# Performance work log

Measured on AMD Instinct MI355X. Metric: run time of the kernel, lower is better.

The kernel has to match this reference:

```python
import jax, jax.numpy as jnp
import numpy as np

COST_CLASS = 1.0
COST_OBJECTNESS = 5.0
COST_GIOU = 2.0
COST_CENTER = 10.0

B, Q, G, C = 32, 1024, 64, 256


def _lsa(cost):
    """Exact rectangular linear sum assignment (Jonker-Volgenant shortest
    augmenting path, same algorithm as scipy.optimize.linear_sum_assignment).
    cost: (R, Cc) float64 numpy array. Returns (row_ind, col_ind), row_ind sorted."""
    transposed = cost.shape[0] > cost.shape[1]
    if transposed:
        cost = cost.T
    n, m = cost.shape
    u = np.zeros(n)
    v = np.zeros(m)
    col4row = np.full(n, -1, dtype=np.int64)
    row4col = np.full(m, -1, dtype=np.int64)
    for cur_row in range(n):
        shortest = np.full(m, np.inf)
        path = np.full(m, -1, dtype=np.int64)
        SC = np.zeros(m, dtype=bool)
        SR_rows = []
        min_val = 0.0
        i = cur_row
        sink = -1
        while sink == -1:
            SR_rows.append(i)
            idx = np.where(~SC)[0]
            r = min_val + cost[i, idx] - u[i] - v[idx]
            better = r < shortest[idx]
            upd = idx[better]
            shortest[upd] = r[better]
            path[upd] = i
            j = idx[np.argmin(shortest[idx])]
            min_val = shortest[j]
            SC[j] = True
            if row4col[j] == -1:
                sink = j
            else:
                i = row4col[j]
        # dual variable update
        u[cur_row] += min_val
        for irow in SR_rows:
            if irow != cur_row:
                u[irow] += min_val - shortest[col4row[irow]]
        v[SC] -= min_val - shortest[SC]
        # augment along the alternating path back to cur_row
        j = sink
        while True:
            i = path[j]
            row4col[j] = i
            col4row[i], j = j, col4row[i]
            if i == cur_row:
                break
    if transposed:
        order = np.argsort(col4row)
        return col4row[order], np.arange(n)[order]
    return np.arange(n), col4row


def setup_inputs() -> dict:
    key = jax.random.key(0)
    k1, k2, k3, k4, k5 = jax.random.split(key, 5)
    return {
        "sem_cls_prob": jax.random.uniform(k1, (B, Q, C), dtype=jnp.float32),
        "objectness_prob": jax.random.uniform(k2, (B, Q), dtype=jnp.float32),
        "center_dist": jax.random.uniform(k3, (B, Q, G), dtype=jnp.float32),
        "gious": jax.random.uniform(k4, (B, Q, G), dtype=jnp.float32),
        "nactual_gt": jax.random.randint(k5, (B,), 0, G, dtype=jnp.int64)
        if jax.config.jax_enable_x64 else jax.random.randint(k5, (B,), 0, G).astype(jnp.int32),
    }


def reference(sem_cls_prob, objectness_prob, center_dist, gious, nactual_gt):
    batchsize, nprop = objectness_prob.shape
    # class_mat == 0 in the original module
    final_cost = (COST_OBJECTNESS * (-objectness_prob[..., None])
                  + COST_CENTER * center_dist
                  + COST_GIOU * (-gious))  # [B, Q, G]
    cost_np = np.asarray(final_cost, dtype=np.float64)
    ngt = np.asarray(nactual_gt)
    per_prop_gt_inds = np.zeros((batchsize, nprop), dtype=np.int64)
    proposal_matched_mask = np.zeros((batchsize, nprop), dtype=np.float32)
    for b in range(batchsize):  # per-batch independent Hungarian (as in source)
        g = int(ngt[b])
        if g > 0:
            rows, cols = _lsa(cost_np[b, :, :g])
            per_prop_gt_inds[b, rows] = cols
            proposal_matched_mask[b, rows] = 1.0
    return jnp.asarray(per_prop_gt_inds), jnp.asarray(proposal_matched_mask)
```

## Files before the change

### kernel.cpp

```cpp
#include <hip/hip_runtime.h>
#include <math.h>

#define B_ 32
#define Q_ 1024
#define G_ 64
#define K16 16

typedef double v16d __attribute__((ext_vector_type(16)));
typedef float  v16f __attribute__((ext_vector_type(16)));
typedef int    v16i __attribute__((ext_vector_type(16)));

#define REP16(OP) OP(0,0) OP(1,1) OP(2,2) OP(3,3) OP(4,4) OP(5,5) OP(6,6) OP(7,7) \
                  OP(8,8) OP(9,9) OP(10,a) OP(11,b) OP(12,c) OP(13,d) OP(14,e) OP(15,f)
#define REP16A(OP,A) OP(A,0,0) OP(A,1,1) OP(A,2,2) OP(A,3,3) OP(A,4,4) OP(A,5,5) OP(A,6,6) OP(A,7,7) \
                     OP(A,8,8) OP(A,9,9) OP(A,10,a) OP(A,11,b) OP(A,12,c) OP(A,13,d) OP(A,14,e) OP(A,15,f)

#define ROR1 0x121
#define ROR2 0x122
#define ROR4 0x124
#define ROR8 0x128
#define BC15 0x142
#define BC31 0x143

template<int CTRL>
__device__ __forceinline__ double dpp_f64(double x) {
    union { double d; int i[2]; } a; a.d = x;
    union { int i[2]; double d; } r;
    r.i[0] = __builtin_amdgcn_update_dpp(a.i[0], a.i[0], CTRL, 0xF, 0xF, false);
    r.i[1] = __builtin_amdgcn_update_dpp(a.i[1], a.i[1], CTRL, 0xF, 0xF, false);
    return r.d;
}
template<int CTRL>
__device__ __forceinline__ int dpp_i32(int x) {
    return __builtin_amdgcn_update_dpp(x, x, CTRL, 0xF, 0xF, false);
}

__device__ __forceinline__ double readlane_f64(double x, int sl) {
    const int s = __builtin_amdgcn_readfirstlane(sl);
    union { double d; int i2[2]; } a; a.d = x;
    union { int i2[2]; double d; } r;
    r.i2[0] = __builtin_amdgcn_readlane(a.i2[0], s);
    r.i2[1] = __builtin_amdgcn_readlane(a.i2[1], s);
    return r.d;
}
__device__ __forceinline__ double readlane_f64c(double x, int sl) {
    union { double d; int i2[2]; } a; a.d = x;
    union { int i2[2]; double d; } r;
    r.i2[0] = __builtin_amdgcn_readlane(a.i2[0], sl);
    r.i2[1] = __builtin_amdgcn_readlane(a.i2[1], sl);
    return r.d;
}
__device__ __forceinline__ float readlane_f32u(float x, int sl) {
    union { float f; int i; } a; a.f = x;
    union { int i; float f; } r;
    r.i = __builtin_amdgcn_readlane(a.i, __builtin_amdgcn_readfirstlane(sl));
    return r.f;
}
__device__ __forceinline__ int readlane_i32(int x, int sl) {
    return __builtin_amdgcn_readlane(x, __builtin_amdgcn_readfirstlane(sl));
}
__device__ __forceinline__ int readlane_i32c(int x, int sl) {
    return __builtin_amdgcn_readlane(x, sl);
}

__device__ __forceinline__ int sel16v_i(v16i p, int s) {
    const int t0_0 = (s & 1) ? p.s1 : p.s0;
    const int t0_1 = (s & 1) ? p.s3 : p.s2;
    const int t0_2 = (s & 1) ? p.s5 : p.s4;
    const int t0_3 = (s & 1) ? p.s7 : p.s6;
    const int t0_4 = (s & 1) ? p.s9 : p.s8;
    const int t0_5 = (s & 1) ? p.sb : p.sa;
    const int t0_6 = (s & 1) ? p.sd : p.sc;
    const int t0_7 = (s & 1) ? p.sf : p.se;
    const int t1_0 = (s & 2) ? t0_1 : t0_0;
    const int t1_1 = (s & 2) ? t0_3 : t0_2;
    const int t1_2 = (s & 2) ? t0_5 : t0_4;
    const int t1_3 = (s & 2) ? t0_7 : t0_6;
    const int a0 = (s & 4) ? t1_1 : t1_0;
    const int a1 = (s & 4) ? t1_3 : t1_2;
    return (s & 8) ? a1 : a0;
}
__device__ __forceinline__ double sel16v_d(v16d p, int s) {
    const double t0_0 = (s & 1) ? p.s1 : p.s0;
    const double t0_1 = (s & 1) ? p.s3 : p.s2;
    const double t0_2 = (s & 1) ? p.s5 : p.s4;
    const double t0_3 = (s & 1) ? p.s7 : p.s6;
    const double t0_4 = (s & 1) ? p.s9 : p.s8;
    const double t0_5 = (s & 1) ? p.sb : p.sa;
    const double t0_6 = (s & 1) ? p.sd : p.sc;
    const double t0_7 = (s & 1) ? p.sf : p.se;
    const double t1_0 = (s & 2) ? t0_1 : t0_0;
    const double t1_1 = (s & 2) ? t0_3 : t0_2;
    const double t1_2 = (s & 2) ? t0_5 : t0_4;
    const double t1_3 = (s & 2) ? t0_7 : t0_6;
    const double a0 = (s & 4) ? t1_1 : t1_0;
    const double a1 = (s & 4) ? t1_3 : t1_2;
    return (s & 8) ? a1 : a0;
}

__device__ __forceinline__ void lexpair(v16d c, int l,
                                        double& gv_o, int& jm_o) {
    bool t;
    t = c.s1 < c.s0; const double p0 = t ? c.s1 : c.s0; const int q0 = t ? 1  : 0;
    t = c.s3 < c.s2; const double p1 = t ? c.s3 : c.s2; const int q1 = t ? 3  : 2;
    t = c.s5 < c.s4; const double p2 = t ? c.s5 : c.s4; const int q2 = t ? 5  : 4;
    t = c.s7 < c.s6; const double p3 = t ? c.s7 : c.s6; const int q3 = t ? 7  : 6;
    t = c.s9 < c.s8; const double p4 = t ? c.s9 : c.s8; const int q4 = t ? 9  : 8;
    t = c.sb < c.sa; const double p5 = t ? c.sb : c.sa; const int q5 = t ? 11 : 10;
    t = c.sd < c.sc; const double p6 = t ? c.sd : c.sc; const int q6 = t ? 13 : 12;
    t = c.sf < c.se; const double p7 = t ? c.sf : c.se; const int q7 = t ? 15 : 14;
    t = p1 < p0; const double r0 = t ? p1 : p0; const int s0 = t ? q1 : q0;
    t = p3 < p2; const double r1 = t ? p3 : p2; const int s1 = t ? q3 : q2;
    t = p5 < p4; const double r2 = t ? p5 : p4; const int s2 = t ? q5 : q4;
    t = p7 < p6; const double r3 = t ? p7 : p6; const int s3 = t ? q7 : q6;
    t = r1 < r0; const double w0 = t ? r1 : r0; const int x0 = t ? s1 : s0;
    t = r3 < r2; const double w1 = t ? r3 : r2; const int x1 = t ? s3 : s2;
    t = w1 < w0; double v = t ? w1 : w0; int key = ((t ? x1 : x0) << 6) | l;
#define LPF_(C) { const double pv = dpp_f64<C>(v); const int pk = dpp_i32<C>(key); \
    const bool tt = (pv < v) || ((pv == v) && (pk < key)); \
    v = tt ? pv : v; key = tt ? pk : key; }
    LPF_(ROR1) LPF_(ROR2) LPF_(ROR4) LPF_(ROR8) LPF_(BC15) LPF_(BC31)
#undef LPF_
    gv_o = readlane_f64c(v, 63);
    jm_o = readlane_i32c(key, 63);
}

__global__ __launch_bounds__(256) void build_kernel(
    const float* __restrict__ obj, const float* __restrict__ cd,
    const float* __restrict__ gi, float* __restrict__ ct,
    float* __restrict__ pv, int* __restrict__ pj,
    float* __restrict__ pv2, int* __restrict__ pj2)
{
    __shared__ float tile[64][65];
    const int b  = blockIdx.x;
    const int cb = blockIdx.y;
    const int jb = cb << 6;
    const int t  = threadIdx.x;
    const float* objb = obj + (b << 10);
    const float4* cd4 = (const float4*)(cd + ((size_t)b << 16));
    const float4* gi4 = (const float4*)(gi + ((size_t)b << 16));

    #pragma unroll
    for (int p = 0; p < 4; ++p) {
        const int f  = t + (p << 8);
        const int jj = f >> 4;
        const int q  = f & 15;
        const int i0 = q << 2;
        const int j  = jb + jj;
        const float om = __fmul_rn(5.0f, -objb[j]);
        const float4 c4 = cd4[(j << 4) + q];
        const float4 q4 = gi4[(j << 4) + q];
        tile[i0 + 0][jj] = __fadd_rn(__fadd_rn(om, __fmul_rn(10.0f, c4.x)), __fmul_rn(2.0f, -q4.x));
        tile[i0 + 1][jj] = __fadd_rn(__fadd_rn(om, __fmul_rn(10.0f, c4.y)), __fmul_rn(2.0f, -q4.y));
        tile[i0 + 2][jj] = __fadd_rn(__fadd_rn(om, __fmul_rn(10.0f, c4.z)), __fmul_rn(2.0f, -q4.z));
        tile[i0 + 3][jj] = __fadd_rn(__fadd_rn(om, __fmul_rn(10.0f, c4.w)), __fmul_rn(2.0f, -q4.w));
    }
    __syncthreads();
    #pragma unroll
    for (int r = 0; r < 16; ++r) {
        const int idx = (r << 8) + t;
        const int i = idx >> 6, j2 = idx & 63;
        ct[(((size_t)(b << 6) + i) << 10) + jb + j2] = tile[i][j2];
    }
    if (t < 64) {
        float bv = tile[t][0]; int bc = 0;
        float sv = 1e30f;      int sc2 = 0;
        #pragma unroll 8
        for (int c = 1; c < 64; ++c) {
            const float v = tile[t][c];
            const bool t1 = v < bv;
            const bool t2 = (!t1) && (v < sv);
            sv  = t1 ? bv : (t2 ? v : sv);
            sc2 = t1 ? bc : (t2 ? c : sc2);
            bv  = t1 ? v : bv;
            bc  = t1 ? c : bc;
        }
        const int o = (((b << 6) + t) << 4) + cb;
        pv[o]  = bv;  pj[o]  = jb + bc;
        pv2[o] = sv;  pj2[o] = jb + sc2;
    }
}

template<class LR>
__device__ __forceinline__ void matcher_core(
    const int l, const int g, LR load_row,
    const float pre_v, const int pre_j, const float sec_v, const int sec_j,
    float* __restrict__ out_ind_b, float* __restrict__ out_mask_b)
{
    const double INF = __builtin_inf();
    double u_rep = 0.0;
    double m_rec = 0.0;
    bool   inSR  = false;
    int    c4r_rep = -1;
    unsigned asg   = 0u;
    unsigned dirty = 0u;
    v16d v_r, sh_r;
    v16i path;
    v16f c_cur, c_i;
#define INI_(K,H) { v_r.s##H = 0.0; sh_r.s##H = 0.0; path.s##H = 0; }
    REP16(INI_)
#undef INI_
#define Z16_(K,H) { c_cur.s##H = 0.0f; c_i.s##H = 0.0f; }
    REP16(Z16_)
#undef Z16_

    for (int cur = 0; cur < g; ++cur) {
        const float pre_vc = readlane_f32u(pre_v, cur);
        int jm = readlane_i32(pre_j, cur);
        double minv = (double)pre_vc;
        bool have_cur = false;
        {
            const int ow1 = jm & 63, sl1 = jm >> 6;
            const unsigned d1 = (unsigned)readlane_i32((int)dirty, ow1);
            if ((d1 >> sl1) & 1u) {
                const float sv_c = readlane_f32u(sec_v, cur);
                const int   sj_c = readlane_i32(sec_j, cur);
                const unsigned d2 = (unsigned)readlane_i32((int)dirty, sj_c & 63);
                if (!((d2 >> (sj_c >> 6)) & 1u) && (sj_c != jm)) {
                    const double vpj = readlane_f64(sel16v_d(v_r, sl1), ow1);
                    const double vA = (double)pre_vc - vpj;
                    const double vB = (double)sv_c;
                    const bool tt = (vB < vA) || ((vB == vA) && (sj_c < jm));
                    minv = tt ? vB : vA;
                    jm   = tt ? sj_c : jm;
                } else {
                    c_cur = load_row(cur); have_cur = true;
                    v16d rr0;
#define RR0_(K,H) rr0.s##H = (double)c_cur.s##H - v_r.s##H;
                    REP16(RR0_)
#undef RR0_
                    lexpair(rr0, l, minv, jm);
                }
            }
        }
        const unsigned long long mk0 = __ballot(c4r_rep == jm);

        if (mk0 == 0ull) {
            u_rep   = (l == cur) ? u_rep + minv : u_rep;
            c4r_rep = (l == cur) ? jm           : c4r_rep;
            asg     = (l == (jm & 63)) ? (asg | (1u << (jm >> 6))) : asg;
        } else {
            if (!have_cur) c_cur = load_row(cur);
            int i = (int)__builtin_ctzll(mk0);
            c_i = load_row(i);
            double ui = readlane_f64(u_rep, i);
            unsigned sc = (l == (jm & 63)) ? (1u << (jm >> 6)) : 0u;
            inSR  = (l == i);
            m_rec = minv;
#define SH0_(K,H) { sh_r.s##H = (double)c_cur.s##H - v_r.s##H; path.s##H = cur; }
            REP16(SH0_)
#undef SH0_

            int sink = -1;
            while (sink < 0) {
                v16d cand;
#define DST_(K,H) { const double rr = ((minv + (double)c_i.s##H) - ui) - v_r.s##H; \
                    const bool notSC = !((sc >> K) & 1u); \
                    const bool upd = notSC && (rr < sh_r.s##H);  \
                    sh_r.s##H = upd ? rr : sh_r.s##H; \
                    path.s##H = upd ? i : path.s##H; \
                    cand.s##H = notSC ? sh_r.s##H : INF; }
                REP16(DST_)
#undef DST_
                lexpair(cand, l, minv, jm);
                const unsigned long long mk = __ballot(c4r_rep == jm);
                if (l == (jm & 63)) sc |= (1u << (jm >> 6));
                if (mk == 0ull) {
                    sink = jm;
                } else {
                    i = (int)__builtin_ctzll(mk);
                    c_i = load_row(i);
                    if (l == i) { inSR = true; m_rec = minv; }
                    ui = readlane_f64(u_rep, i);
                }
            }

            if (l == cur)       u_rep += minv;
            else if (inSR)      u_rep += minv - m_rec;
            unsigned chg = 0u;
#define VUP_(K,H) { const bool in_sc = (sc >> K) & 1u; \
                    const double nv = v_r.s##H - (minv - sh_r.s##H); \
                    chg = (in_sc && (sh_r.s##H != minv)) ? (chg | (1u << K)) : chg; \
                    v_r.s##H = in_sc ? nv : v_r.s##H; }
            REP16(VUP_)
#undef VUP_
            dirty |= chg;

            int j = sink;
            while (true) {
                const int so = j & 63, ss = j >> 6;
                const int ii = readlane_i32(sel16v_i(path, ss), so);
                const int nj = readlane_i32(c4r_rep, ii);
                asg     = (l == so) ? (asg | (1u << ss)) : asg;
                c4r_rep = (l == ii) ? j : c4r_rep;
                j = nj;
                if (ii == cur) break;
            }
        }
    }

#define OUT_(K,H) { const int jj = l + (K << 6); const bool a_ = (asg >> K) & 1u; \
    out_mask_b[jj] = a_ ? 1.0f : 0.0f; \
    if (!a_) out_ind_b[jj] = 0.0f; }
    REP16(OUT_)
#undef OUT_
    if (c4r_rep >= 0) out_ind_b[c4r_rep] = (float)l;
}

__global__ __launch_bounds__(64, 1) void matcher_ws(
    const int* __restrict__ ngt, const float* __restrict__ ct,
    const float* __restrict__ pv, const int* __restrict__ pj,
    const float* __restrict__ pv2, const int* __restrict__ pj2,
    float* __restrict__ out_ind, float* __restrict__ out_mask)
{
    const int b = blockIdx.x;
    const int l = threadIdx.x;
    const int g = ngt[b];
    const float* ctb = ct + ((size_t)(b << 6) << 10);

    const int base = ((b << 6) + l) << 4;
    const float4* pvq = (const float4*)(pv  + base);
    const int4*   pjq = (const int4*)(pj  + base);
    const float4* svq = (const float4*)(pv2 + base);
    const int4*   sjq = (const int4*)(pj2 + base);
    const float4 pA = pvq[0], pB = pvq[1], pC = pvq[2], pD = pvq[3];
    const int4   jA = pjq[0], jB = pjq[1], jC = pjq[2], jD = pjq[3];
    const float4 sA = svq[0], sB = svq[1], sC = svq[2], sD = svq[3];
    const int4   tA = sjq[0], tB = sjq[1], tC = sjq[2], tD = sjq[3];
    float bv = pA.x; int bj = jA.x; float sv = sA.x; int sj = tA.x;
#define MERGE_(CV,CJ,C2V,C2J) { const bool nb = (CV) < bv; \
    const bool s1 = (C2V) < bv; const bool s2 = (CV) < sv; \
    const float nsv = nb ? (s1 ? (C2V) : bv) : (s2 ? (CV) : sv); \
    const int   nsj = nb ? (s1 ? (C2J) : bj) : (s2 ? (CJ) : sj); \
    bj = nb ? (CJ) : bj; bv = nb ? (CV) : bv; sv = nsv; sj = nsj; }
    MERGE_(pA.y,jA.y,sA.y,tA.y) MERGE_(pA.z,jA.z,sA.z,tA.z) MERGE_(pA.w,jA.w,sA.w,tA.w)
    MERGE_(pB.x,jB.x,sB.x,tB.x) MERGE_(pB.y,jB.y,sB.y,tB.y) MERGE_(pB.z,jB.z,sB.z,tB.z) MERGE_(pB.w,jB.w,sB.w,tB.w)
    MERGE_(pC.x,jC.x,sC.x,tC.x) MERGE_(pC.y,jC.y,sC.y,tC.y) MERGE_(pC.z,jC.z,sC.z,tC.z) MERGE_(pC.w,jC.w,sC.w,tC.w)
    MERGE_(pD.x,jD.x,sD.x,tD.x) MERGE_(pD.y,jD.y,sD.y,tD.y) MERGE_(pD.z,jD.z,sD.z,tD.z) MERGE_(pD.w,jD.w,sD.w,tD.w)
#undef MERGE_

    auto load_row = [&](int ri) -> v16f {
        v16f d; const float* rp_ = ctb + ((size_t)ri << 10) + l;
#define LDW_(D,K,H) D.s##H = rp_[(K) << 6];
        REP16A(LDW_, d)
#undef LDW_
        return d;
    };
    matcher_core(l, g, load_row, bv, bj, sv, sj,
                 out_ind + (b << 10), out_mask + (b << 10));
}

__global__ __launch_bounds__(64, 1) void matcher_nws(
    const float* __restrict__ obj, const float* __restrict__ cd,
    const float* __restrict__ gi, const int* __restrict__ ngt,
    float* __restrict__ out_ind, float* __restrict__ out_mask)
{
    const int b = blockIdx.x;
    const int l = threadIdx.x;
    const int g = ngt[b];
    const float* objb = obj + (b << 10);
    const float* cdb  = cd + ((size_t)b << 16);
    const float* gib  = gi + ((size_t)b << 16);

    v16f objm;
#define OBJI_(K,H) objm.s##H = __fmul_rn(5.0f, -objb[l + (K << 6)]);
    REP16(OBJI_)
#undef OBJI_
    auto load_row = [&](int ri) -> v16f {
        v16f d;
#define LDN_(D,K,H) { const int idx_ = ((l + ((K) << 6)) << 6) + ri; \
    D.s##H = __fadd_rn(__fadd_rn(objm.s##H, __fmul_rn(10.0f, cdb[idx_])), \
                       __fmul_rn(2.0f, -gib[idx_])); }
        REP16A(LDN_, d)
#undef LDN_
        return d;
    };

    float pre_v = 0.0f; int pre_j = 0;
    for (int i = 0; i < g; ++i) {
        v16f c = load_row(i);
        v16d c64;
#define CV_(K,H) c64.s##H = (double)c.s##H;
        REP16(CV_)
#undef CV_
        double gv; int j0;
        lexpair(c64, l, gv, j0);
        pre_v = (l == i) ? (float)gv : pre_v;
        pre_j = (l == i) ? j0 : pre_j;
    }
    matcher_core(l, g, load_row, pre_v, pre_j, pre_v, pre_j,
                 out_ind + (b << 10), out_mask + (b << 10));
}

extern "C" void kernel_launch(void* const* d_in, const int* in_sizes, int n_in,
                              void* d_out, int out_size, void* d_ws, size_t ws_size,
                              hipStream_t stream)
{
    const float* obj = (const float*)d_in[1];
    const float* cd  = (const float*)d_in[2];
    const float* gi  = (const float*)d_in[3];
    const int*   ngt = (const int*)d_in[4];
    float* out0 = (float*)d_out;
    float* out1 = out0 + B_ * Q_;

    const size_t ct_b = (size_t)B_ * G_ * Q_ * sizeof(float);
    const size_t pv_b = (size_t)B_ * G_ * 16 * sizeof(float);
    if (ws_size >= ct_b + 4 * pv_b) {
        float* ct  = (float*)d_ws;
        float* pv  = (float*)((char*)d_ws + ct_b);
        int*   pj  = (int*)  ((char*)d_ws + ct_b + pv_b);
        float* pv2 = (float*)((char*)d_ws + ct_b + 2 * pv_b);
        int*   pj2 = (int*)  ((char*)d_ws + ct_b + 3 * pv_b);
        build_kernel<<<dim3(B_, 16), 256, 0, stream>>>(obj, cd, gi, ct, pv, pj, pv2, pj2);
        matcher_ws<<<B_, 64, 0, stream>>>(ngt, ct, pv, pj, pv2, pj2, out0, out1);
    } else {
        matcher_nws<<<B_, 64, 0, stream>>>(obj, cd, gi, ngt, out0, out1);
    }
}
```

Baseline: 162.5 us.

## Split lexicographic argmin reduction, reorder build grid, add cache-warming waves in matcher

The fused value-and-key DPP reduction is replaced by a value-only fmin wave reduction, after which lanes holding the minimum recover their local index and a second integer-only reduction picks the lowest key. The build grid is transposed so consecutive blocks cover the same batch. The matcher launches 256 threads, and the extra three waves stream the batch's cost table through loads whose results are discarded, to warm the cache for the serial single-wave Hungarian loop. The warming waves take CU resources and bandwidth, and fmin behaves differently from the original comparisons on NaN.

```diff
diff --git a/kernel.cpp b/kernel.cpp
--- a/kernel.cpp
+++ b/kernel.cpp
@@ -100,29 +100,34 @@
 
 __device__ __forceinline__ void lexpair(v16d c, int l,
                                         double& gv_o, int& jm_o) {
-    bool t;
-    t = c.s1 < c.s0; const double p0 = t ? c.s1 : c.s0; const int q0 = t ? 1  : 0;
-    t = c.s3 < c.s2; const double p1 = t ? c.s3 : c.s2; const int q1 = t ? 3  : 2;
-    t = c.s5 < c.s4; const double p2 = t ? c.s5 : c.s4; const int q2 = t ? 5  : 4;
-    t = c.s7 < c.s6; const double p3 = t ? c.s7 : c.s6; const int q3 = t ? 7  : 6;
-    t = c.s9 < c.s8; const double p4 = t ? c.s9 : c.s8; const int q4 = t ? 9  : 8;
-    t = c.sb < c.sa; const double p5 = t ? c.sb : c.sa; const int q5 = t ? 11 : 10;
-    t = c.sd < c.sc; const double p6 = t ? c.sd : c.sc; const int q6 = t ? 13 : 12;
-    t = c.sf < c.se; const double p7 = t ? c.sf : c.se; const int q7 = t ? 15 : 14;
-    t = p1 < p0; const double r0 = t ? p1 : p0; const int s0 = t ? q1 : q0;
-    t = p3 < p2; const double r1 = t ? p3 : p2; const int s1 = t ? q3 : q2;
-    t = p5 < p4; const double r2 = t ? p5 : p4; const int s2 = t ? q5 : q4;
-    t = p7 < p6; const double r3 = t ? p7 : p6; const int s3 = t ? q7 : q6;
-    t = r1 < r0; const double w0 = t ? r1 : r0; const int x0 = t ? s1 : s0;
-    t = r3 < r2; const double w1 = t ? r3 : r2; const int x1 = t ? s3 : s2;
-    t = w1 < w0; double v = t ? w1 : w0; int key = ((t ? x1 : x0) << 6) | l;
-#define LPF_(C) { const double pv = dpp_f64<C>(v); const int pk = dpp_i32<C>(key); \
-    const bool tt = (pv < v) || ((pv == v) && (pk < key)); \
-    v = tt ? pv : v; key = tt ? pk : key; }
-    LPF_(ROR1) LPF_(ROR2) LPF_(ROR4) LPF_(ROR8) LPF_(BC15) LPF_(BC31)
-#undef LPF_
-    gv_o = readlane_f64c(v, 63);
+    const double a0 = fmin(c.s0, c.s1), a1 = fmin(c.s2, c.s3),
+                 a2 = fmin(c.s4, c.s5), a3 = fmin(c.s6, c.s7),
+                 a4 = fmin(c.s8, c.s9), a5 = fmin(c.sa, c.sb),
+                 a6 = fmin(c.sc, c.sd), a7 = fmin(c.se, c.sf);
+    const double b0 = fmin(a0, a1), b1 = fmin(a2, a3),
+                 b2 = fmin(a4, a5), b3 = fmin(a6, a7);
+    const double d0 = fmin(b0, b1), d1 = fmin(b2, b3);
+    const double vloc = fmin(d0, d1);
+    double v = vloc;
+#define VS_(C) { const double pv = dpp_f64<C>(v); v = fmin(pv, v); }
+    VS_(ROR1) VS_(ROR2) VS_(ROR4) VS_(ROR8) VS_(BC15) VS_(BC31)
+#undef VS_
+    const double gv = readlane_f64c(v, 63);
+    const int bit3 = (d0 == gv) ? 0 : 1;
+    const double bsel = bit3 ? b2 : b0;
+    const int bit2 = (bsel == gv) ? 0 : 1;
+    const double asel = bit2 ? (bit3 ? a6 : a2) : (bit3 ? a4 : a0);
+    const int bit1 = (asel == gv) ? 0 : 1;
+    const double csel = bit1 ? (bit2 ? (bit3 ? c.se : c.s6) : (bit3 ? c.sa : c.s2))
+                             : (bit2 ? (bit3 ? c.sc : c.s4) : (bit3 ? c.s8 : c.s0));
+    const int bit0 = (csel == gv) ? 0 : 1;
+    const int kloc = (bit3 << 3) | (bit2 << 2) | (bit1 << 1) | bit0;
+    int key = (vloc == gv) ? ((kloc << 6) | l) : 0x7FFFFFFF;
+#define KS_(C) { const int pk = dpp_i32<C>(key); key = (pk < key) ? pk : key; }
+    KS_(ROR1) KS_(ROR2) KS_(ROR4) KS_(ROR8) KS_(BC15) KS_(BC31)
+#undef KS_
     jm_o = readlane_i32c(key, 63);
+    gv_o = gv;
 }
 
 __global__ __launch_bounds__(256) void build_kernel(
@@ -132,9 +137,8 @@
     float* __restrict__ pv2, int* __restrict__ pj2)
 {
     __shared__ float tile[64][65];
-    const int b  = blockIdx.x;
-    const int cb = blockIdx.y;
-    const int jb = cb << 6;
+    const int b  = blockIdx.y;
+    const int jb = blockIdx.x << 6;
     const int t  = threadIdx.x;
     const float* objb = obj + (b << 10);
     const float4* cd4 = (const float4*)(cd + ((size_t)b << 16));
@@ -175,7 +179,7 @@
             bv  = t1 ? v : bv;
             bc  = t1 ? c : bc;
         }
-        const int o = (((b << 6) + t) << 4) + cb;
+        const int o = (((b << 6) + t) << 4) + blockIdx.x;
         pv[o]  = bv;  pj[o]  = jb + bc;
         pv2[o] = sv;  pj2[o] = jb + sc2;
     }
@@ -307,16 +311,27 @@
     if (c4r_rep >= 0) out_ind_b[c4r_rep] = (float)l;
 }
 
-__global__ __launch_bounds__(64, 1) void matcher_ws(
+__global__ __launch_bounds__(256, 1) void matcher_ws(
     const int* __restrict__ ngt, const float* __restrict__ ct,
     const float* __restrict__ pv, const int* __restrict__ pj,
     const float* __restrict__ pv2, const int* __restrict__ pj2,
     float* __restrict__ out_ind, float* __restrict__ out_mask)
 {
     const int b = blockIdx.x;
-    const int l = threadIdx.x;
+    const int t = threadIdx.x;
+    const float* ctb = ct + ((size_t)(b << 6) << 10);
+
+    if (t >= 64) {
+        const float4* c4p = (const float4*)ctb;
+        for (int n = t - 64; n < 16384; n += 192) {
+            const float4 x = c4p[n];
+            asm volatile("" :: "v"(x.x), "v"(x.y), "v"(x.z), "v"(x.w));
+        }
+        return;
+    }
+
+    const int l = t;
     const int g = ngt[b];
-    const float* ctb = ct + ((size_t)(b << 6) << 10);
 
     const int base = ((b << 6) + l) << 4;
     const float4* pvq = (const float4*)(pv  + base);
@@ -411,8 +426,8 @@
         int*   pj  = (int*)  ((char*)d_ws + ct_b + pv_b);
         float* pv2 = (float*)((char*)d_ws + ct_b + 2 * pv_b);
         int*   pj2 = (int*)  ((char*)d_ws + ct_b + 3 * pv_b);
-        build_kernel<<<dim3(B_, 16), 256, 0, stream>>>(obj, cd, gi, ct, pv, pj, pv2, pj2);
-        matcher_ws<<<B_, 64, 0, stream>>>(ngt, ct, pv, pj, pv2, pj2, out0, out1);
+        build_kernel<<<dim3(16, B_), 256, 0, stream>>>(obj, cd, gi, ct, pv, pj, pv2, pj2);
+        matcher_ws<<<B_, 256, 0, stream>>>(ngt, ct, pv, pj, pv2, pj2, out0, out1);
     } else {
         matcher_nws<<<B_, 64, 0, stream>>>(obj, cd, gi, ngt, out0, out1);
     }
```

Measured after the change: 156.7 us. 3.5% less time.
